# Kernel tuning notes

Hardware: AMD Instinct MI355X
Metric: run time of the kernel (lower is better)

The kernel has to match this reference:

```python
import jax, jax.numpy as jnp
import numpy as np

NOISE = 0.1
B, CI, CO, NS, NPTS = 2, 64, 64, 16, 1024
P = B * NS * NPTS  # total per-point noise draws = 32768


def setup_inputs() -> dict:
    key = jax.random.key(0)
    k1, k2, k3, k4 = jax.random.split(key, 4)
    x = jax.random.normal(k1, (B, CI, NS, NPTS), dtype=jnp.float32)
    W = jax.random.normal(k2, (CO, CI), dtype=jnp.float32) * 0.05  # conv.weight[:, :, 0, 0]
    b = jax.random.normal(k3, (CO,), dtype=jnp.float32) * 0.05    # conv.bias (never noised)
    eps = jax.random.normal(k4, (P, CO, CI), dtype=jnp.float32)   # randn_like(weight) per point
    return {"x": x, "W": W, "b": b, "eps": eps}


def reference(x, W, b, eps):
    Bn, Ci, ns, npts = x.shape
    # Faithful to torch: x.reshape(1, in_features, 1, -1) on a [B,Ci,ns,np] tensor
    # (row-major flatten then re-chunk by Ci, which interleaves batch into points).
    xf = x.reshape(Ci, -1)  # [Ci, P]
    # per-point noised weight: W_p = W * (1 + NOISE * eps[p]); bias is shared, un-noised
    base = jnp.einsum('oi,ip->op', W, xf)                      # [CO, P]
    noisy = NOISE * jnp.einsum('poi,oi,ip->op', eps, W, xf)    # [CO, P]
    y = base + noisy + b[:, None]
    return y.reshape(Bn, CO, ns, npts)
```

## Files before the change

kernel.cpp:

```cpp
#include <hip/hip_runtime.h>
#include <cstddef>

constexpr int P_TOTAL = 32768;
constexpr int NCH     = 64;
constexpr int PPB     = 32;
constexpr int PPW     = 8;
constexpr int XPAD    = 68;

__global__ __launch_bounds__(256) void noise_conv_kernel(
    const float* __restrict__ x, const float* __restrict__ W,
    const float* __restrict__ bias, const float* __restrict__ eps,
    float* __restrict__ out)
{
    __shared__ __align__(16) float4 Wl[NCH * NCH / 4];
    __shared__ __align__(16) float  xt[PPB][XPAD];

    const int tid  = threadIdx.x;
    const int lane = tid & 63;
    const int wv   = tid >> 6;
    const int p0   = blockIdx.x * PPB;
    const int g    = lane >> 4;
    const int s    = lane & 15;

    const float4* W4 = reinterpret_cast<const float4*>(W);
#pragma unroll
    for (int c = 0; c < 4; ++c) {
        int idx = c * 256 + tid;
        Wl[idx] = W4[idx];
    }
#pragma unroll
    for (int c = 0; c < (PPB * NCH) / 256; ++c) {
        int e = c * 256 + tid;
        int i = e >> 5;
        int j = e & (PPB - 1);
        xt[j][i] = x[i * P_TOTAL + p0 + j];
    }

    const int   o_fin = 4 * s + g;
    const float b_fin = bias[o_fin];

    __syncthreads();

    const int jj0 = wv * PPW;
    const float4* ep_base = reinterpret_cast<const float4*>(eps)
                          + (size_t)(p0 + jj0) * (NCH * NCH / 4) + lane;

    float4 eA[8], eB[8];
#pragma unroll
    for (int k = 0; k < 8; ++k) eA[k] = ep_base[k * 64];

    for (int j = 0; j < PPW; ++j) {
        const int jj = jj0 + j;
        const int p  = p0 + jj;
        const float4* ep4 = ep_base + (size_t)j * (NCH * NCH / 4);

#pragma unroll
        for (int k = 0; k < 8; ++k) eB[k] = ep4[(k + 8) * 64];

        const float4 x4 = *reinterpret_cast<const float4*>(&xt[jj][4 * s]);

        float acc[16];
#pragma unroll
        for (int k = 0; k < 8; ++k) {
            float4 w4 = Wl[k * 64 + lane];
            float wx0 = w4.x * x4.x, wx1 = w4.y * x4.y;
            float wx2 = w4.z * x4.z, wx3 = w4.w * x4.w;
            float f0 = fmaf(0.1f, eA[k].x, 1.0f);
            float f1 = fmaf(0.1f, eA[k].y, 1.0f);
            float f2 = fmaf(0.1f, eA[k].z, 1.0f);
            float f3 = fmaf(0.1f, eA[k].w, 1.0f);
            float a  = wx0 * f0;
            a = fmaf(wx1, f1, a);
            a = fmaf(wx2, f2, a);
            a = fmaf(wx3, f3, a);
            acc[k] = a;
        }

        if (j + 1 < PPW) {
            const float4* epn = ep_base + (size_t)(j + 1) * (NCH * NCH / 4);
#pragma unroll
            for (int k = 0; k < 8; ++k) eA[k] = epn[k * 64];
        }

#pragma unroll
        for (int k = 8; k < 16; ++k) {
            float4 w4 = Wl[k * 64 + lane];
            float wx0 = w4.x * x4.x, wx1 = w4.y * x4.y;
            float wx2 = w4.z * x4.z, wx3 = w4.w * x4.w;
            float4 e4 = eB[k - 8];
            float f0 = fmaf(0.1f, e4.x, 1.0f);
            float f1 = fmaf(0.1f, e4.y, 1.0f);
            float f2 = fmaf(0.1f, e4.z, 1.0f);
            float f3 = fmaf(0.1f, e4.w, 1.0f);
            float a  = wx0 * f0;
            a = fmaf(wx1, f1, a);
            a = fmaf(wx2, f2, a);
            a = fmaf(wx3, f3, a);
            acc[k] = a;
        }

        float r8[8];
#pragma unroll
        for (int t = 0; t < 8; ++t) {
            float mine  = (s & 8) ? acc[t + 8] : acc[t];
            float other = (s & 8) ? acc[t]     : acc[t + 8];
            r8[t] = mine + __shfl_xor(other, 8, 64);
        }
        float r4[4];
#pragma unroll
        for (int t = 0; t < 4; ++t) {
            float mine  = (s & 4) ? r8[t + 4] : r8[t];
            float other = (s & 4) ? r8[t]     : r8[t + 4];
            r4[t] = mine + __shfl_xor(other, 4, 64);
        }
        float r2[2];
#pragma unroll
        for (int t = 0; t < 2; ++t) {
            float mine  = (s & 2) ? r4[t + 2] : r4[t];
            float other = (s & 2) ? r4[t]     : r4[t + 2];
            r2[t] = mine + __shfl_xor(other, 2, 64);
        }
        {
            float mine  = (s & 1) ? r2[1] : r2[0];
            float other = (s & 1) ? r2[0] : r2[1];
            float y = mine + __shfl_xor(other, 1, 64) + b_fin;
            out[(size_t)o_fin * P_TOTAL + p] = y;
        }
    }
}

extern "C" void kernel_launch(void* const* d_in, const int* in_sizes, int n_in,
                              void* d_out, int out_size, void* d_ws, size_t ws_size,
                              hipStream_t stream) {
    const float* x    = (const float*)d_in[0];
    const float* W    = (const float*)d_in[1];
    const float* bias = (const float*)d_in[2];
    const float* eps  = (const float*)d_in[3];
    float* out        = (float*)d_out;

    dim3 grid(P_TOTAL / PPB);
    dim3 block(256);
    noise_conv_kernel<<<grid, block, 0, stream>>>(x, W, bias, eps, out);
}
```

Baseline: 697.6 us.

## Shrink blocks, stream eps with nontemporal rotating loads, vectorize output stores

Halves points per block and per wave, so more blocks are launched, and adds a minimum-occupancy launch bound. The cross-iteration prefetch of eps is replaced by a rotating two-buffer scheme of 4-vector chunks within each point, read with nontemporal loads to keep the one-shot stream out of the cache. Each thread now buffers its four outputs and writes them as one nontemporal float4 store instead of four scalar stores. This targets memory-bound streaming of the large eps tensor, at the cost of less lookahead across points and more per-block overhead for loading W.

Measured after the change: 837.5 us. +20.1%, slower.

```diff
diff --git a/kernel.cpp b/kernel.cpp
--- a/kernel.cpp
+++ b/kernel.cpp
@@ -3,17 +3,20 @@
 
 constexpr int P_TOTAL = 32768;
 constexpr int NCH     = 64;
-constexpr int PPB     = 32;
-constexpr int PPW     = 8;
+constexpr int PPB     = 16;
+constexpr int PPW     = 4;
 constexpr int XPAD    = 68;
 
-__global__ __launch_bounds__(256) void noise_conv_kernel(
+
+using vf4 = __attribute__((ext_vector_type(4))) float;
+
+__global__ __launch_bounds__(256, 5) void noise_conv_kernel(
     const float* __restrict__ x, const float* __restrict__ W,
     const float* __restrict__ bias, const float* __restrict__ eps,
     float* __restrict__ out)
 {
-    __shared__ __align__(16) float4 Wl[NCH * NCH / 4];
-    __shared__ __align__(16) float  xt[PPB][XPAD];
+    __shared__ __align__(16) vf4   Wl[NCH * NCH / 4];
+    __shared__ __align__(16) float xt[PPB][XPAD];
 
     const int tid  = threadIdx.x;
     const int lane = tid & 63;
@@ -22,7 +25,7 @@
     const int g    = lane >> 4;
     const int s    = lane & 15;
 
-    const float4* W4 = reinterpret_cast<const float4*>(W);
+    const vf4* W4 = reinterpret_cast<const vf4*>(W);
 #pragma unroll
     for (int c = 0; c < 4; ++c) {
         int idx = c * 256 + tid;
@@ -31,7 +34,7 @@
 #pragma unroll
     for (int c = 0; c < (PPB * NCH) / 256; ++c) {
         int e = c * 256 + tid;
-        int i = e >> 5;
+        int i = e >> 4;
         int j = e & (PPB - 1);
         xt[j][i] = x[i * P_TOTAL + p0 + j];
     }
@@ -42,52 +45,91 @@
     __syncthreads();
 
     const int jj0 = wv * PPW;
-    const float4* ep_base = reinterpret_cast<const float4*>(eps)
-                          + (size_t)(p0 + jj0) * (NCH * NCH / 4) + lane;
+    const vf4* ep_base = reinterpret_cast<const vf4*>(eps)
+                       + (size_t)(p0 + jj0) * (NCH * NCH / 4) + lane;
 
-    float4 eA[8], eB[8];
+    float y4[PPW];
+
 #pragma unroll
-    for (int k = 0; k < 8; ++k) eA[k] = ep_base[k * 64];
-
     for (int j = 0; j < PPW; ++j) {
         const int jj = jj0 + j;
-        const int p  = p0 + jj;
-        const float4* ep4 = ep_base + (size_t)j * (NCH * NCH / 4);
+        const vf4* ep4 = ep_base + (size_t)j * (NCH * NCH / 4);
+
+        const vf4 x4 = *reinterpret_cast<const vf4*>(&xt[jj][4 * s]);
+
+        float acc[16];
+        vf4 ea[4], eb[4];
 
 #pragma unroll
-        for (int k = 0; k < 8; ++k) eB[k] = ep4[(k + 8) * 64];
+        for (int t = 0; t < 4; ++t)
+            ea[t] = __builtin_nontemporal_load(ep4 + t * 64);
+#pragma unroll
+        for (int t = 0; t < 4; ++t)
+            eb[t] = __builtin_nontemporal_load(ep4 + (4 + t) * 64);
 
-        const float4 x4 = *reinterpret_cast<const float4*>(&xt[jj][4 * s]);
-
-        float acc[16];
 #pragma unroll
-        for (int k = 0; k < 8; ++k) {
-            float4 w4 = Wl[k * 64 + lane];
+        for (int t = 0; t < 4; ++t) {
+            vf4 w4 = Wl[t * 64 + lane];
+            vf4 e4 = ea[t];
             float wx0 = w4.x * x4.x, wx1 = w4.y * x4.y;
             float wx2 = w4.z * x4.z, wx3 = w4.w * x4.w;
-            float f0 = fmaf(0.1f, eA[k].x, 1.0f);
-            float f1 = fmaf(0.1f, eA[k].y, 1.0f);
-            float f2 = fmaf(0.1f, eA[k].z, 1.0f);
-            float f3 = fmaf(0.1f, eA[k].w, 1.0f);
+            float f0 = fmaf(0.1f, e4.x, 1.0f);
+            float f1 = fmaf(0.1f, e4.y, 1.0f);
+            float f2 = fmaf(0.1f, e4.z, 1.0f);
+            float f3 = fmaf(0.1f, e4.w, 1.0f);
+            float a  = wx0 * f0;
+            a = fmaf(wx1, f1, a);
+            a = fmaf(wx2, f2, a);
+            a = fmaf(wx3, f3, a);
+            acc[t] = a;
+        }
+#pragma unroll
+        for (int t = 0; t < 4; ++t)
+            ea[t] = __builtin_nontemporal_load(ep4 + (8 + t) * 64);
+#pragma unroll
+        for (int t = 0; t < 4; ++t) {
+            int k = 4 + t;
+            vf4 w4 = Wl[k * 64 + lane];
+            vf4 e4 = eb[t];
+            float wx0 = w4.x * x4.x, wx1 = w4.y * x4.y;
+            float wx2 = w4.z * x4.z, wx3 = w4.w * x4.w;
+            float f0 = fmaf(0.1f, e4.x, 1.0f);
+            float f1 = fmaf(0.1f, e4.y, 1.0f);
+            float f2 = fmaf(0.1f, e4.z, 1.0f);
+            float f3 = fmaf(0.1f, e4.w, 1.0f);
             float a  = wx0 * f0;
             a = fmaf(wx1, f1, a);
             a = fmaf(wx2, f2, a);
             a = fmaf(wx3, f3, a);
             acc[k] = a;
         }
-
-        if (j + 1 < PPW) {
-            const float4* epn = ep_base + (size_t)(j + 1) * (NCH * NCH / 4);
 #pragma unroll
-            for (int k = 0; k < 8; ++k) eA[k] = epn[k * 64];
-        }
-
+        for (int t = 0; t < 4; ++t)
+            eb[t] = __builtin_nontemporal_load(ep4 + (12 + t) * 64);
 #pragma unroll
-        for (int k = 8; k < 16; ++k) {
-            float4 w4 = Wl[k * 64 + lane];
+        for (int t = 0; t < 4; ++t) {
+            int k = 8 + t;
+            vf4 w4 = Wl[k * 64 + lane];
+            vf4 e4 = ea[t];
             float wx0 = w4.x * x4.x, wx1 = w4.y * x4.y;
             float wx2 = w4.z * x4.z, wx3 = w4.w * x4.w;
-            float4 e4 = eB[k - 8];
+            float f0 = fmaf(0.1f, e4.x, 1.0f);
+            float f1 = fmaf(0.1f, e4.y, 1.0f);
+            float f2 = fmaf(0.1f, e4.z, 1.0f);
+            float f3 = fmaf(0.1f, e4.w, 1.0f);
+            float a  = wx0 * f0;
+            a = fmaf(wx1, f1, a);
+            a = fmaf(wx2, f2, a);
+            a = fmaf(wx3, f3, a);
+            acc[k] = a;
+        }
+#pragma unroll
+        for (int t = 0; t < 4; ++t) {
+            int k = 12 + t;
+            vf4 w4 = Wl[k * 64 + lane];
+            vf4 e4 = eb[t];
+            float wx0 = w4.x * x4.x, wx1 = w4.y * x4.y;
+            float wx2 = w4.z * x4.z, wx3 = w4.w * x4.w;
             float f0 = fmaf(0.1f, e4.x, 1.0f);
             float f1 = fmaf(0.1f, e4.y, 1.0f);
             float f2 = fmaf(0.1f, e4.z, 1.0f);
@@ -123,10 +165,14 @@
         {
             float mine  = (s & 1) ? r2[1] : r2[0];
             float other = (s & 1) ? r2[0] : r2[1];
-            float y = mine + __shfl_xor(other, 1, 64) + b_fin;
-            out[(size_t)o_fin * P_TOTAL + p] = y;
+            y4[j] = mine + __shfl_xor(other, 1, 64) + b_fin;
         }
     }
+
+    vf4 yv;
+    yv.x = y4[0]; yv.y = y4[1]; yv.z = y4[2]; yv.w = y4[3];
+    __builtin_nontemporal_store(
+        yv, reinterpret_cast<vf4*>(&out[(size_t)o_fin * P_TOTAL + p0 + jj0]));
 }
 
 extern "C" void kernel_launch(void* const* d_in, const int* in_sizes, int n_in,
```

## Split output channels across waves and keep W slice in registers

Applied to the files above, without the earlier changes.

Reassigns work so each wave owns 16 output channels across all 16 points of a block, rather than all 64 channels for 8 points. Each wave's slice of W now lives in registers, replacing the shared-memory copy, and the eps loads are double-buffered through a fully unrolled 16-step pipeline. Outputs are written as float4 vector stores from four lanes, and the shuffle reduction gets shorter. The kernel is bound by streaming the 512MB eps tensor, so the gain depends mainly on whether there are enough loads in flight. Halving points per block doubles the grid and repeats the W and x setup more often.

Result: no change. 688.2 us (-1.3%).

```diff
diff --git a/kernel.cpp b/kernel.cpp
--- a/kernel.cpp
+++ b/kernel.cpp
@@ -3,130 +3,119 @@
 
 constexpr int P_TOTAL = 32768;
 constexpr int NCH     = 64;
-constexpr int PPB     = 32;
-constexpr int PPW     = 8;
+constexpr int PPB     = 16;
 constexpr int XPAD    = 68;
+
+
+using vf4 = __attribute__((ext_vector_type(4))) float;
+
+__device__ __forceinline__ float dot4(vf4 w4, vf4 x4, vf4 e4) {
+    float f0 = fmaf(0.1f, e4.x, 1.0f);
+    float f1 = fmaf(0.1f, e4.y, 1.0f);
+    float f2 = fmaf(0.1f, e4.z, 1.0f);
+    float f3 = fmaf(0.1f, e4.w, 1.0f);
+    float a  = (w4.x * x4.x) * f0;
+    a = fmaf(w4.y * x4.y, f1, a);
+    a = fmaf(w4.z * x4.z, f2, a);
+    a = fmaf(w4.w * x4.w, f3, a);
+    return a;
+}
 
 __global__ __launch_bounds__(256) void noise_conv_kernel(
     const float* __restrict__ x, const float* __restrict__ W,
     const float* __restrict__ bias, const float* __restrict__ eps,
     float* __restrict__ out)
 {
-    __shared__ __align__(16) float4 Wl[NCH * NCH / 4];
-    __shared__ __align__(16) float  xt[PPB][XPAD];
+    __shared__ __align__(16) float xt[PPB][XPAD];
 
     const int tid  = threadIdx.x;
     const int lane = tid & 63;
-    const int wv   = tid >> 6;
-    const int p0   = blockIdx.x * PPB;
+    const int w    = tid >> 6;
     const int g    = lane >> 4;
     const int s    = lane & 15;
+    const int p0   = blockIdx.x * PPB;
 
-    const float4* W4 = reinterpret_cast<const float4*>(W);
-#pragma unroll
-    for (int c = 0; c < 4; ++c) {
-        int idx = c * 256 + tid;
-        Wl[idx] = W4[idx];
-    }
 #pragma unroll
     for (int c = 0; c < (PPB * NCH) / 256; ++c) {
         int e = c * 256 + tid;
-        int i = e >> 5;
+        int i = e >> 4;
         int j = e & (PPB - 1);
         xt[j][i] = x[i * P_TOTAL + p0 + j];
     }
 
-    const int   o_fin = 4 * s + g;
+    const vf4* W4 = reinterpret_cast<const vf4*>(W);
+    const vf4 Wr0 = W4[256 * w +   0 + lane];
+    const vf4 Wr1 = W4[256 * w +  64 + lane];
+    const vf4 Wr2 = W4[256 * w + 128 + lane];
+    const vf4 Wr3 = W4[256 * w + 192 + lane];
+
+    const int   o_fin = 16 * w + 4 * (s & 3) + g;
     const float b_fin = bias[o_fin];
 
     __syncthreads();
 
-    const int jj0 = wv * PPW;
-    const float4* ep_base = reinterpret_cast<const float4*>(eps)
-                          + (size_t)(p0 + jj0) * (NCH * NCH / 4) + lane;
+    const vf4* ebase = reinterpret_cast<const vf4*>(eps)
+                     + (size_t)p0 * 1024 + 256 * w + lane;
 
-    float4 eA[8], eB[8];
-#pragma unroll
-    for (int k = 0; k < 8; ++k) eA[k] = ep_base[k * 64];
+    vf4 eA0, eA1, eA2, eA3, eB0, eB1, eB2, eB3;
+    float y0, y1, y2, y3;
 
-    for (int j = 0; j < PPW; ++j) {
-        const int jj = jj0 + j;
-        const int p  = p0 + jj;
-        const float4* ep4 = ep_base + (size_t)j * (NCH * NCH / 4);
+#define LOADQ(E0, E1, E2, E3, J) do {                                   \
+        const vf4* _ep = ebase + (size_t)(J) * 1024;                     \
+        E0 = _ep[0]; E1 = _ep[64]; E2 = _ep[128]; E3 = _ep[192];         \
+    } while (0)
 
-#pragma unroll
-        for (int k = 0; k < 8; ++k) eB[k] = ep4[(k + 8) * 64];
+#define COMPUTE(J, E0, E1, E2, E3, Y) do {                               \
+        const vf4 x4 = *reinterpret_cast<const vf4*>(&xt[(J)][4 * s]);   \
+        float a0 = dot4(Wr0, x4, E0);                                    \
+        float a1 = dot4(Wr1, x4, E1);                                    \
+        float a2 = dot4(Wr2, x4, E2);                                    \
+        float a3 = dot4(Wr3, x4, E3);                                    \
+        a0 += __shfl_xor(a0, 8, 64); a1 += __shfl_xor(a1, 8, 64);        \
+        a2 += __shfl_xor(a2, 8, 64); a3 += __shfl_xor(a3, 8, 64);        \
+        a0 += __shfl_xor(a0, 4, 64); a1 += __shfl_xor(a1, 4, 64);        \
+        a2 += __shfl_xor(a2, 4, 64); a3 += __shfl_xor(a3, 4, 64);        \
+        float c0 = (s & 2) ? a2 : a0, d0 = (s & 2) ? a0 : a2;            \
+        float c1 = (s & 2) ? a3 : a1, d1 = (s & 2) ? a1 : a3;            \
+        c0 += __shfl_xor(d0, 2, 64); c1 += __shfl_xor(d1, 2, 64);        \
+        float m  = (s & 1) ? c1 : c0, dd = (s & 1) ? c0 : c1;            \
+        Y = m + __shfl_xor(dd, 1, 64) + b_fin;                           \
+    } while (0)
 
-        const float4 x4 = *reinterpret_cast<const float4*>(&xt[jj][4 * s]);
+#define STOREB(BASE) do {                                                \
+        if (s < 4) {                                                     \
+            vf4 yv; yv.x = y0; yv.y = y1; yv.z = y2; yv.w = y3;          \
+            *reinterpret_cast<vf4*>(                                     \
+                &out[(size_t)o_fin * P_TOTAL + p0 + (BASE)]) = yv;       \
+        }                                                                \
+    } while (0)
 
-        float acc[16];
-#pragma unroll
-        for (int k = 0; k < 8; ++k) {
-            float4 w4 = Wl[k * 64 + lane];
-            float wx0 = w4.x * x4.x, wx1 = w4.y * x4.y;
-            float wx2 = w4.z * x4.z, wx3 = w4.w * x4.w;
-            float f0 = fmaf(0.1f, eA[k].x, 1.0f);
-            float f1 = fmaf(0.1f, eA[k].y, 1.0f);
-            float f2 = fmaf(0.1f, eA[k].z, 1.0f);
-            float f3 = fmaf(0.1f, eA[k].w, 1.0f);
-            float a  = wx0 * f0;
-            a = fmaf(wx1, f1, a);
-            a = fmaf(wx2, f2, a);
-            a = fmaf(wx3, f3, a);
-            acc[k] = a;
-        }
+    LOADQ(eA0, eA1, eA2, eA3, 0);
 
-        if (j + 1 < PPW) {
-            const float4* epn = ep_base + (size_t)(j + 1) * (NCH * NCH / 4);
-#pragma unroll
-            for (int k = 0; k < 8; ++k) eA[k] = epn[k * 64];
-        }
+    LOADQ(eB0, eB1, eB2, eB3, 1);  COMPUTE(0,  eA0, eA1, eA2, eA3, y0);
+    LOADQ(eA0, eA1, eA2, eA3, 2);  COMPUTE(1,  eB0, eB1, eB2, eB3, y1);
+    LOADQ(eB0, eB1, eB2, eB3, 3);  COMPUTE(2,  eA0, eA1, eA2, eA3, y2);
+    LOADQ(eA0, eA1, eA2, eA3, 4);  COMPUTE(3,  eB0, eB1, eB2, eB3, y3);
+    STOREB(0);
+    LOADQ(eB0, eB1, eB2, eB3, 5);  COMPUTE(4,  eA0, eA1, eA2, eA3, y0);
+    LOADQ(eA0, eA1, eA2, eA3, 6);  COMPUTE(5,  eB0, eB1, eB2, eB3, y1);
+    LOADQ(eB0, eB1, eB2, eB3, 7);  COMPUTE(6,  eA0, eA1, eA2, eA3, y2);
+    LOADQ(eA0, eA1, eA2, eA3, 8);  COMPUTE(7,  eB0, eB1, eB2, eB3, y3);
+    STOREB(4);
+    LOADQ(eB0, eB1, eB2, eB3, 9);  COMPUTE(8,  eA0, eA1, eA2, eA3, y0);
+    LOADQ(eA0, eA1, eA2, eA3, 10); COMPUTE(9,  eB0, eB1, eB2, eB3, y1);
+    LOADQ(eB0, eB1, eB2, eB3, 11); COMPUTE(10, eA0, eA1, eA2, eA3, y2);
+    LOADQ(eA0, eA1, eA2, eA3, 12); COMPUTE(11, eB0, eB1, eB2, eB3, y3);
+    STOREB(8);
+    LOADQ(eB0, eB1, eB2, eB3, 13); COMPUTE(12, eA0, eA1, eA2, eA3, y0);
+    LOADQ(eA0, eA1, eA2, eA3, 14); COMPUTE(13, eB0, eB1, eB2, eB3, y1);
+    LOADQ(eB0, eB1, eB2, eB3, 15); COMPUTE(14, eA0, eA1, eA2, eA3, y2);
+                                   COMPUTE(15, eB0, eB1, eB2, eB3, y3);
+    STOREB(12);
 
-#pragma unroll
-        for (int k = 8; k < 16; ++k) {
-            float4 w4 = Wl[k * 64 + lane];
-            float wx0 = w4.x * x4.x, wx1 = w4.y * x4.y;
-            float wx2 = w4.z * x4.z, wx3 = w4.w * x4.w;
-            float4 e4 = eB[k - 8];
-            float f0 = fmaf(0.1f, e4.x, 1.0f);
-            float f1 = fmaf(0.1f, e4.y, 1.0f);
-            float f2 = fmaf(0.1f, e4.z, 1.0f);
-            float f3 = fmaf(0.1f, e4.w, 1.0f);
-            float a  = wx0 * f0;
-            a = fmaf(wx1, f1, a);
-            a = fmaf(wx2, f2, a);
-            a = fmaf(wx3, f3, a);
-            acc[k] = a;
-        }
-
-        float r8[8];
-#pragma unroll
-        for (int t = 0; t < 8; ++t) {
-            float mine  = (s & 8) ? acc[t + 8] : acc[t];
-            float other = (s & 8) ? acc[t]     : acc[t + 8];
-            r8[t] = mine + __shfl_xor(other, 8, 64);
-        }
-        float r4[4];
-#pragma unroll
-        for (int t = 0; t < 4; ++t) {
-            float mine  = (s & 4) ? r8[t + 4] : r8[t];
-            float other = (s & 4) ? r8[t]     : r8[t + 4];
-            r4[t] = mine + __shfl_xor(other, 4, 64);
-        }
-        float r2[2];
-#pragma unroll
-        for (int t = 0; t < 2; ++t) {
-            float mine  = (s & 2) ? r4[t + 2] : r4[t];
-            float other = (s & 2) ? r4[t]     : r4[t + 2];
-            r2[t] = mine + __shfl_xor(other, 2, 64);
-        }
-        {
-            float mine  = (s & 1) ? r2[1] : r2[0];
-            float other = (s & 1) ? r2[0] : r2[1];
-            float y = mine + __shfl_xor(other, 1, 64) + b_fin;
-            out[(size_t)o_fin * P_TOTAL + p] = y;
-        }
-    }
+#undef LOADQ
+#undef COMPUTE
+#undef STOREB
 }
 
 extern "C" void kernel_launch(void* const* d_in, const int* in_sizes, int n_in,
```
